# Optimization experiments

Hardware: AMD Instinct MI355X
Metric: run time of the kernel (lower is better)

The kernel has to match this reference:

```python
import jax, jax.numpy as jnp
import numpy as np

B, N, HD = 4, 2048, 256
E, T = 4096, 1024
PROPAG_STEPS = 5
ALPHA_MAX = 0.2
LN_EPS = 1e-5


def setup_inputs() -> dict:
    key = jax.random.key(0)
    ks = jax.random.split(key, 16)
    s_in, s_h = (2.0 * HD) ** -0.5, HD ** -0.5
    return {
        "attr_matrix": jax.random.normal(ks[0], (B, N, 1), dtype=jnp.float32),
        "adj_matrix": jax.random.uniform(ks[1], (B, N, N), dtype=jnp.float32),
        # ggnn.linear_i: 1 -> HD
        "W_i": jax.random.normal(ks[2], (HD, 1), dtype=jnp.float32),
        "b_i": jnp.zeros((HD,), dtype=jnp.float32),
        # ggnn.gru: GRUCell(input=2*HD, hidden=HD), torch gate order r,z,n
        "W_ih": jax.random.normal(ks[3], (3 * HD, 2 * HD), dtype=jnp.float32) * s_in,
        "b_ih": jnp.zeros((3 * HD,), dtype=jnp.float32),
        "W_hh": jax.random.normal(ks[4], (3 * HD, HD), dtype=jnp.float32) * s_h,
        "b_hh": jnp.zeros((3 * HD,), dtype=jnp.float32),
        # ggnn.linear_o: HD -> 1
        "W_o": jax.random.normal(ks[5], (1, HD), dtype=jnp.float32) * s_h,
        "b_o": jnp.zeros((1,), dtype=jnp.float32),
        # topo buffers (incidence-like, kept small to mimic sparse +/-1 matrices)
        "B1": jax.random.normal(ks[6], (N, E), dtype=jnp.float32) * 0.02,
        "B2": jax.random.normal(ks[7], (E, T), dtype=jnp.float32) * 0.02,
        # topo trainables
        "proj_W": jax.random.normal(ks[8], (HD, HD), dtype=jnp.float32) * s_h,
        "ln_gamma": jnp.ones((HD,), dtype=jnp.float32),
        "ln_beta": jnp.zeros((HD,), dtype=jnp.float32),
        "alpha_raw": jnp.float32(-2.0),
    }


def _gru_cell(x, h, W_ih, b_ih, W_hh, b_hh):
    # x: [B,N,2H], h: [B,N,H]; torch GRUCell gate order: r, z, n
    gx = jnp.einsum('bni,gi->bng', x, W_ih) + b_ih
    gh = jnp.einsum('bnh,gh->bng', h, W_hh) + b_hh
    xr, xz, xn = jnp.split(gx, 3, axis=-1)
    hr, hz, hn = jnp.split(gh, 3, axis=-1)
    r = jax.nn.sigmoid(xr + hr)
    z = jax.nn.sigmoid(xz + hz)
    n = jnp.tanh(xn + r * hn)
    return (1.0 - z) * n + z * h


def _layernorm(x, gamma, beta):
    mu = jnp.mean(x, axis=-1, keepdims=True)
    var = jnp.mean(jnp.square(x - mu), axis=-1, keepdims=True)
    return (x - mu) * jax.lax.rsqrt(var + LN_EPS) * gamma + beta


def reference(attr_matrix, adj_matrix, W_i, b_i, W_ih, b_ih, W_hh, b_hh,
              W_o, b_o, B1, B2, proj_W, ln_gamma, ln_beta, alpha_raw):
    A_in = adj_matrix                      # [B,N,N]
    A_out = jnp.swapaxes(adj_matrix, -2, -1)
    # linear_i + relu
    h = jax.nn.relu(jnp.einsum('bnc,hc->bnh', attr_matrix, W_i) + b_i)  # [B,N,H]
    # GGNN propagation
    for _ in range(PROPAG_STEPS):
        a_in = jnp.einsum('bnm,bmh->bnh', A_in, h)
        a_out = jnp.einsum('bnm,bmh->bnh', A_out, h)
        h = _gru_cell(jnp.concatenate((a_in, a_out), axis=-1), h,
                      W_ih, b_ih, W_hh, b_hh)
    # topo residual: dH = B1 (L1 (B1^T h)), L1 = B1^T B1 + B2 B2^T
    L1 = B1.T @ B1 + B2 @ B2.T             # [E,E]
    E_feat = jnp.einsum('ne,bnh->beh', B1, h)       # B1^T H
    E_topo = jnp.einsum('ef,bfh->beh', L1, E_feat)
    dH = jnp.einsum('ne,beh->bnh', B1, E_topo)
    dH = _layernorm(jax.nn.relu(jnp.einsum('bnh,oh->bno', dH, proj_W)),
                    ln_gamma, ln_beta)
    alpha = ALPHA_MAX * jax.nn.sigmoid(alpha_raw)
    h = h + alpha * dH
    # linear_o -> [B,N] (squeeze(0) is a no-op for B>1)
    anomaly = (jnp.einsum('bnh,oh->bno', h, W_o) + b_o)[..., 0]
    return anomaly
```

## Files before the change

### kernel.cpp

```cpp
#include <hip/hip_runtime.h>
#include <hip/hip_fp16.h>


typedef __bf16 bf16x8 __attribute__((ext_vector_type(8)));
typedef _Float16 f16x8 __attribute__((ext_vector_type(8)));
typedef float f32x4 __attribute__((ext_vector_type(4)));

#define BM 128
#define BN 128
#define BK 16
#define LO_INV (1.f / 1024.f)

__device__ __forceinline__ unsigned short bf16rne(float x)
{
    unsigned u = __float_as_uint(x);
    return (unsigned short)((u + 0x7FFFu + ((u >> 16) & 1u)) >> 16);
}
__device__ __forceinline__ float bf2f(unsigned short h)
{
    return __uint_as_float((unsigned)h << 16);
}
__device__ __forceinline__ void split2(float x, unsigned short& hi, unsigned short& lo)
{
    hi = bf16rne(x);
    lo = bf16rne(x - bf2f(hi));
}

__device__ __forceinline__ unsigned short f16r(float x)
{
    return __half_as_ushort(__float2half(x));
}
__device__ __forceinline__ float f16f(unsigned short u)
{
    return __half2float(__ushort_as_half(u));
}
__device__ __forceinline__ void splitf(float x, unsigned short& hi, unsigned short& lo)
{
    hi = f16r(x);
    lo = f16r((x - f16f(hi)) * 1024.f);
}

__device__ __forceinline__ void gload_lds16(const unsigned short* g, unsigned short* l)
{
    __builtin_amdgcn_global_load_lds(
        (const __attribute__((address_space(1))) void*)g,
        (__attribute__((address_space(3))) void*)l, 16, 0, 0);
}

__device__ __forceinline__ void stage2(const unsigned short* g, unsigned short* l, int ld)
{
    gload_lds16(g, l);
    gload_lds16(g + (size_t)32 * ld, l + 2048);
}

template<int SPLIT>
__device__ __forceinline__ void mm_loop64f(
    const unsigned short* ag0, const unsigned short* ag1,
    const unsigned short* bg0, const unsigned short* bg1,
    int K, int lda, int ldb, unsigned short* LDS, int tid,
    f32x4 (&acc0)[2][2], f32x4 (&acc1)[2][2])
{
    constexpr int NT = SPLIT ? 2 : 1;
    constexpr int TSZ = 4096;

    int lane = tid & 63, r16 = lane & 15, g = lane >> 4, s7 = r16 & 7;
    int wv = tid >> 6, wr = wv >> 1, wc = wv & 1;
    int arow = (wr * 32 + r16) * 128;
    int brow = (wc * 32 + r16) * 128;
    unsigned short* lA = LDS + (tid >> 6) * 512;
    unsigned short* lB = LDS + NT * TSZ + (tid >> 6) * 512;
    const char* Ab = (const char*)LDS;
    const char* Bb = (const char*)(LDS + NT * TSZ);

    for (int k0 = 0; k0 < K; k0 += 64) {
        stage2(ag0 + k0, lA, lda);
        if constexpr (SPLIT) stage2(ag1 + k0, lA + TSZ, lda);
        stage2(bg0 + k0, lB, ldb);
        if constexpr (SPLIT) stage2(bg1 + k0, lB + TSZ, ldb);
        __syncthreads();
#pragma unroll
        for (int ks = 0; ks < 2; ++ks) {
            int tt = ((ks * 4 + g) ^ s7) * 16;
            f16x8 a0[2], a1[2], b0[2], b1[2];
#pragma unroll
            for (int mi = 0; mi < 2; ++mi) {
                a0[mi] = *(const f16x8*)(Ab + arow + mi * 2048 + tt);
                if constexpr (SPLIT)
                    a1[mi] = *(const f16x8*)(Ab + TSZ * 2 + arow + mi * 2048 + tt);
            }
#pragma unroll
            for (int ni = 0; ni < 2; ++ni) {
                b0[ni] = *(const f16x8*)(Bb + brow + ni * 2048 + tt);
                if constexpr (SPLIT)
                    b1[ni] = *(const f16x8*)(Bb + TSZ * 2 + brow + ni * 2048 + tt);
            }
#pragma unroll
            for (int mi = 0; mi < 2; ++mi)
#pragma unroll
                for (int ni = 0; ni < 2; ++ni) {
                    if constexpr (SPLIT) {
                        acc1[mi][ni] = __builtin_amdgcn_mfma_f32_16x16x32_f16(
                            a1[mi], b0[ni], acc1[mi][ni], 0, 0, 0);
                        acc1[mi][ni] = __builtin_amdgcn_mfma_f32_16x16x32_f16(
                            a0[mi], b1[ni], acc1[mi][ni], 0, 0, 0);
                    }
                    acc0[mi][ni] = __builtin_amdgcn_mfma_f32_16x16x32_f16(
                        a0[mi], b0[ni], acc0[mi][ni], 0, 0, 0);
                }
        }
        __syncthreads();
    }
}

template<int SPLIT, int OF16>
__global__ __launch_bounds__(256, 2) void mm_f16(
    const unsigned short* __restrict__ Ah, const unsigned short* __restrict__ Al,
    int lda,
    const unsigned short* __restrict__ Bh, const unsigned short* __restrict__ Bl,
    int ldb,
    int K, const float* __restrict__ bias, const float* __restrict__ Cacc,
    void* __restrict__ Cout, int ldc)
{
    constexpr int NT = SPLIT ? 2 : 1;
    __shared__ unsigned short LDS[2 * NT * 4096];
    int tid = threadIdx.x;

    unsigned nwg = gridDim.x * gridDim.y;
    unsigned lin = blockIdx.y * gridDim.x + blockIdx.x;
    unsigned wk = ((nwg & 7) == 0) ? (lin & 7) * (nwg >> 3) + (lin >> 3) : lin;
    unsigned bx = wk % gridDim.x, by = wk / gridDim.x;

    int m0 = by * 64, n0 = bx * 64;
    int rp = tid >> 3, sl8 = ((tid & 7) ^ (rp & 7)) * 8;
    const unsigned short* ag0 = Ah + (size_t)(m0 + rp) * lda + sl8;
    const unsigned short* ag1 = SPLIT ? Al + (size_t)(m0 + rp) * lda + sl8 : nullptr;
    const unsigned short* bg0 = Bh + (size_t)(n0 + rp) * ldb + sl8;
    const unsigned short* bg1 = SPLIT ? Bl + (size_t)(n0 + rp) * ldb + sl8 : nullptr;

    f32x4 acc0[2][2], acc1[2][2];
#pragma unroll
    for (int mi = 0; mi < 2; ++mi)
#pragma unroll
        for (int ni = 0; ni < 2; ++ni) {
            acc0[mi][ni] = (f32x4){0.f, 0.f, 0.f, 0.f};
            acc1[mi][ni] = (f32x4){0.f, 0.f, 0.f, 0.f};
        }

    mm_loop64f<SPLIT>(ag0, ag1, bg0, bg1, K, lda, ldb, LDS, tid, acc0, acc1);

    int lane = tid & 63, r16 = lane & 15, g = lane >> 4;
    int wv = tid >> 6, wr = wv >> 1, wc = wv & 1;
#pragma unroll
    for (int mi = 0; mi < 2; ++mi) {
#pragma unroll
        for (int ni = 0; ni < 2; ++ni) {
            int col = n0 + wc * 32 + ni * 16 + r16;
            float badd = bias ? bias[col] : 0.f;
#pragma unroll
            for (int j = 0; j < 4; ++j) {
                int row = m0 + wr * 32 + mi * 16 + g * 4 + j;
                float v = acc0[mi][ni][j] + badd;
                if (SPLIT) v += acc1[mi][ni][j] * LO_INV;
                if (Cacc) v += Cacc[(size_t)row * ldc + col];
                if (OF16)
                    ((unsigned short*)Cout)[(size_t)row * ldc + col] = f16r(v);
                else
                    ((float*)Cout)[(size_t)row * ldc + col] = v;
            }
        }
    }
}

__global__ __launch_bounds__(256, 2) void gxgru(
    const unsigned short* __restrict__ Xhi, const unsigned short* __restrict__ Xlo,
    const unsigned short* __restrict__ WihH, const unsigned short* __restrict__ WihL,
    const float* __restrict__ b_ih, const float* __restrict__ ghb,
    float* __restrict__ h,
    unsigned short* __restrict__ hrmh, unsigned short* __restrict__ hrml,
    unsigned short* __restrict__ hTh, unsigned short* __restrict__ hTl)
{
    __shared__ unsigned short LDS[34816];
    int tid = threadIdx.x;

    unsigned lin = blockIdx.y * 4 + blockIdx.x;
    unsigned wk = (lin & 7) * 64 + (lin >> 3);
    unsigned tb = wk & 3, by = wk >> 2;

    int m0 = by * 64;
    const int K = 512;
    int rp = tid >> 3, sl8 = ((tid & 7) ^ (rp & 7)) * 8;
    const unsigned short* ag0 = Xhi + (size_t)(m0 + rp) * K + sl8;
    const unsigned short* ag1 = Xlo + (size_t)(m0 + rp) * K + sl8;
    const unsigned short* bh0 = WihH + (size_t)(tb * 192 + rp) * K + sl8;
    const unsigned short* bl0 = WihL + (size_t)(tb * 192 + rp) * K + sl8;

    int lane = tid & 63, r16 = lane & 15, lg = lane >> 4, s7 = r16 & 7;
    int wv = tid >> 6, wr = wv >> 1, wc = wv & 1;
    int arow = (wr * 32 + r16) * 128;
    int brow = (wc * 32 + r16) * 128;
    unsigned short* lA = LDS + (tid >> 6) * 512;
    unsigned short* lB = LDS + 8192 + (tid >> 6) * 512;

    f32x4 acc0[3][2][2], acc1[3][2][2];
#pragma unroll
    for (int g = 0; g < 3; ++g)
#pragma unroll
        for (int mi = 0; mi < 2; ++mi)
#pragma unroll
            for (int ni = 0; ni < 2; ++ni) {
                acc0[g][mi][ni] = (f32x4){0.f, 0.f, 0.f, 0.f};
                acc1[g][mi][ni] = (f32x4){0.f, 0.f, 0.f, 0.f};
            }

    for (int k0 = 0; k0 < K; k0 += 64) {
        stage2(ag0 + k0, lA, K);
        stage2(ag1 + k0, lA + 4096, K);
#pragma unroll
        for (int g = 0; g < 3; ++g) {
            stage2(bh0 + (size_t)(g * 64) * K + k0, lB + g * 4096, K);
            stage2(bl0 + (size_t)(g * 64) * K + k0, lB + 12288 + g * 4096, K);
        }
        __syncthreads();
#pragma unroll
        for (int ks = 0; ks < 2; ++ks) {
            int tt = ((ks * 4 + lg) ^ s7) * 16;
            f16x8 a0[2], a1[2];
#pragma unroll
            for (int mi = 0; mi < 2; ++mi) {
                a0[mi] = *(const f16x8*)((const char*)LDS + arow + mi * 2048 + tt);
                a1[mi] = *(const f16x8*)((const char*)LDS + 8192 + arow + mi * 2048 + tt);
            }
#pragma unroll
            for (int g = 0; g < 3; ++g) {
                f16x8 b0[2], b1[2];
#pragma unroll
                for (int ni = 0; ni < 2; ++ni) {
                    b0[ni] = *(const f16x8*)((const char*)LDS + 16384 + g * 8192 +
                                             brow + ni * 2048 + tt);
                    b1[ni] = *(const f16x8*)((const char*)LDS + 40960 + g * 8192 +
                                             brow + ni * 2048 + tt);
                }
#pragma unroll
                for (int mi = 0; mi < 2; ++mi)
#pragma unroll
                    for (int ni = 0; ni < 2; ++ni) {
                        acc1[g][mi][ni] = __builtin_amdgcn_mfma_f32_16x16x32_f16(
                            a1[mi], b0[ni], acc1[g][mi][ni], 0, 0, 0);
                        acc1[g][mi][ni] = __builtin_amdgcn_mfma_f32_16x16x32_f16(
                            a0[mi], b1[ni], acc1[g][mi][ni], 0, 0, 0);
                        acc0[g][mi][ni] = __builtin_amdgcn_mfma_f32_16x16x32_f16(
                            a0[mi], b0[ni], acc0[g][mi][ni], 0, 0, 0);
                    }
            }
        }
        __syncthreads();
    }

    float* T2 = reinterpret_cast<float*>(LDS);
#pragma unroll
    for (int mi = 0; mi < 2; ++mi) {
#pragma unroll
        for (int ni = 0; ni < 2; ++ni) {
            int tl = wc * 32 + ni * 16 + r16;
            int t = tb * 64 + tl;
            float br = b_ih[t], bz = b_ih[256 + t], bn = b_ih[512 + t];
#pragma unroll
            for (int j = 0; j < 4; ++j) {
                int rl = wr * 32 + mi * 16 + lg * 4 + j;
                int row = m0 + rl;
                float xr = acc0[0][mi][ni][j] + acc1[0][mi][ni][j] * LO_INV + br;
                float xz = acc0[1][mi][ni][j] + acc1[1][mi][ni][j] * LO_INV + bz;
                float xn = acc0[2][mi][ni][j] + acc1[2][mi][ni][j] * LO_INV + bn;
                size_t grow = (size_t)row * 768;
                float hr = ghb[grow + t];
                float hz = ghb[grow + 256 + t];
                float hn = ghb[grow + 512 + t];
                float r = 1.f / (1.f + __expf(-(xr + hr)));
                float z = 1.f / (1.f + __expf(-(xz + hz)));
                float nn = tanhf(xn + r * hn);
                size_t hix = (size_t)row * 256 + t;
                T2[rl * 68 + tl] = (1.f - z) * nn + z * h[hix];
            }
        }
    }
    __syncthreads();

    {
        int rl = tid >> 2, tq = tid & 3;
        const float* src = T2 + rl * 68 + tq * 16;
        int row = m0 + rl;
        int tbase = tb * 64 + tq * 16;
        unsigned hw[8], lw[8];
#pragma unroll
        for (int e = 0; e < 8; ++e) {
            unsigned short h0, l0, h1, l1;
            splitf(src[2 * e], h0, l0);
            splitf(src[2 * e + 1], h1, l1);
            hw[e] = (unsigned)h0 | ((unsigned)h1 << 16);
            lw[e] = (unsigned)l0 | ((unsigned)l1 << 16);
        }
        float* hd = h + (size_t)row * 256 + tbase;
#pragma unroll
        for (int q = 0; q < 4; ++q)
            ((float4*)hd)[q] = *(const float4*)(src + q * 4);
        size_t ro = (size_t)row * 256 + tbase;
        ((uint4*)(hrmh + ro))[0] = (uint4){hw[0], hw[1], hw[2], hw[3]};
        ((uint4*)(hrmh + ro))[1] = (uint4){hw[4], hw[5], hw[6], hw[7]};
        ((uint4*)(hrml + ro))[0] = (uint4){lw[0], lw[1], lw[2], lw[3]};
        ((uint4*)(hrml + ro))[1] = (uint4){lw[4], lw[5], lw[6], lw[7]};
    }

    {
        int b = tid >> 6, tl = tid & 63;
        int f = b * 256 + tb * 64 + tl;
        int nbase = m0 >> 2;
        unsigned hw[8], lw[8];
#pragma unroll
        for (int e = 0; e < 8; ++e) {
            float x0 = T2[(4 * (2 * e) + b) * 68 + tl];
            float x1 = T2[(4 * (2 * e + 1) + b) * 68 + tl];
            unsigned short h0, l0, h1, l1;
            splitf(x0, h0, l0);
            splitf(x1, h1, l1);
            hw[e] = (unsigned)h0 | ((unsigned)h1 << 16);
            lw[e] = (unsigned)l0 | ((unsigned)l1 << 16);
        }
        size_t fo = (size_t)f * 2048 + nbase;
        ((uint4*)(hTh + fo))[0] = (uint4){hw[0], hw[1], hw[2], hw[3]};
        ((uint4*)(hTh + fo))[1] = (uint4){hw[4], hw[5], hw[6], hw[7]};
        ((uint4*)(hTl + fo))[0] = (uint4){lw[0], lw[1], lw[2], lw[3]};
        ((uint4*)(hTl + fo))[1] = (uint4){lw[4], lw[5], lw[6], lw[7]};
    }
}

__global__ __launch_bounds__(256, 2) void mm_step1f(
    const unsigned short* __restrict__ AhHi, const unsigned short* __restrict__ AhLo,
    const unsigned short* __restrict__ AtHi, const unsigned short* __restrict__ AtLo,
    const unsigned short* __restrict__ hTh, const unsigned short* __restrict__ hTl,
    unsigned short* __restrict__ Xhi, unsigned short* __restrict__ Xlo,
    const unsigned short* __restrict__ hrmh, const unsigned short* __restrict__ hrml,
    const unsigned short* __restrict__ WhhH, const unsigned short* __restrict__ WhhL,
    const float* __restrict__ b_hh, float* __restrict__ ghb)
{
    __shared__ unsigned short LDS[16384];
    int tid = threadIdx.x;
    unsigned bid = blockIdx.x;
    int lane = tid & 63, r16 = lane & 15, g = lane >> 4;
    int wv = tid >> 6, wr = wv >> 1, wc = wv & 1;
    int rp = tid >> 3, sl8 = ((tid & 7) ^ (rp & 7)) * 8;

    f32x4 acc0[2][2], acc1[2][2];
#pragma unroll
    for (int mi = 0; mi < 2; ++mi)
#pragma unroll
        for (int ni = 0; ni < 2; ++ni) {
            acc0[mi][ni] = (f32x4){0.f, 0.f, 0.f, 0.f};
            acc1[mi][ni] = (f32x4){0.f, 0.f, 0.f, 0.f};
        }

    if (bid < 1024) {
        unsigned wk = (bid & 7) * 128 + (bid >> 3);
        unsigned bz = wk >> 7, rem = wk & 127, by = rem >> 2, bx = rem & 3;
        int b = bz >> 1, wio = bz & 1;
        const unsigned short* Ahp = (wio ? AtHi : AhHi) + (size_t)b * 4194304;
        const unsigned short* Alp = (wio ? AtLo : AhLo) + (size_t)b * 4194304;
        size_t boff = (size_t)(b * 256 + bx * 64) * 2048;
        int m0 = by * 64;
        const int K = 2048;
        const unsigned short* ag0 = Ahp + (size_t)(m0 + rp) * K + sl8;
        const unsigned short* ag1 = Alp + (size_t)(m0 + rp) * K + sl8;
        const unsigned short* bg0 = hTh + boff + (size_t)rp * K + sl8;
        const unsigned short* bg1 = hTl + boff + (size_t)rp * K + sl8;

        mm_loop64f<1>(ag0, ag1, bg0, bg1, K, K, K, LDS, tid, acc0, acc1);

        float* T = reinterpret_cast<float*>(LDS);
#pragma unroll
        for (int mi = 0; mi < 2; ++mi)
#pragma unroll
            for (int ni = 0; ni < 2; ++ni)
#pragma unroll
                for (int j = 0; j < 4; ++j)
                    T[(wr * 32 + mi * 16 + g * 4 + j) * 68 +
                      wc * 32 + ni * 16 + r16] =
                        acc0[mi][ni][j] + acc1[mi][ni][j] * LO_INV;
        __syncthreads();

        int row = tid >> 2, fq = tid & 3;
        const float* src = T + row * 68 + fq * 16;
        unsigned hw[8], lw[8];
#pragma unroll
        for (int e = 0; e < 8; ++e) {
            unsigned short h0, l0, h1, l1;
            splitf(src[2 * e], h0, l0);
            splitf(src[2 * e + 1], h1, l1);
            hw[e] = (unsigned)h0 | ((unsigned)h1 << 16);
            lw[e] = (unsigned)l0 | ((unsigned)l1 << 16);
        }
        size_t base = ((size_t)(m0 + row) * 4 + b) * 512 + wio * 256 + bx * 64 + fq * 16;
        ((uint4*)(Xhi + base))[0] = (uint4){hw[0], hw[1], hw[2], hw[3]};
        ((uint4*)(Xhi + base))[1] = (uint4){hw[4], hw[5], hw[6], hw[7]};
        ((uint4*)(Xlo + base))[0] = (uint4){lw[0], lw[1], lw[2], lw[3]};
        ((uint4*)(Xlo + base))[1] = (uint4){lw[4], lw[5], lw[6], lw[7]};
    } else {
        unsigned gidx = bid - 1024;
        unsigned by = gidx / 12, bx = gidx % 12;
        int m0 = by * 64, n0 = bx * 64;
        const int K = 256;
        const unsigned short* ag0 = hrmh + (size_t)(m0 + rp) * K + sl8;
        const unsigned short* ag1 = hrml + (size_t)(m0 + rp) * K + sl8;
        const unsigned short* bg0 = WhhH + (size_t)(n0 + rp) * K + sl8;
        const unsigned short* bg1 = WhhL + (size_t)(n0 + rp) * K + sl8;

        mm_loop64f<1>(ag0, ag1, bg0, bg1, K, K, K, LDS, tid, acc0, acc1);

#pragma unroll
        for (int mi = 0; mi < 2; ++mi) {
#pragma unroll
            for (int ni = 0; ni < 2; ++ni) {
                int col = n0 + wc * 32 + ni * 16 + r16;
                float badd = b_hh[col];
#pragma unroll
                for (int j = 0; j < 4; ++j) {
                    int row = m0 + wr * 32 + mi * 16 + g * 4 + j;
                    ghb[(size_t)row * 768 + col] =
                        acc0[mi][ni][j] + acc1[mi][ni][j] * LO_INV + badd;
                }
            }
        }
    }
}

__global__ void split_adj16(const float* __restrict__ adj,
                            unsigned short* __restrict__ nhi, unsigned short* __restrict__ nlo,
                            unsigned short* __restrict__ thi, unsigned short* __restrict__ tlo)
{
    __shared__ float t[64][68];
    int z = blockIdx.z;
    const float* src = adj + (size_t)z * 4194304;
    int tx = threadIdx.x & 15, ty = threadIdx.x >> 4;
    int i0 = blockIdx.y * 64, j0 = blockIdx.x * 64;
#pragma unroll
    for (int i = 0; i < 4; ++i) {
        int r = ty * 4 + i;
        float4 v = *(const float4*)(src + (size_t)(i0 + r) * 2048 + j0 + tx * 4);
        ushort4 h, l;
        splitf(v.x, h.x, l.x); splitf(v.y, h.y, l.y);
        splitf(v.z, h.z, l.z); splitf(v.w, h.w, l.w);
        size_t o = (size_t)z * 4194304 + (size_t)(i0 + r) * 2048 + j0 + tx * 4;
        *(ushort4*)(nhi + o) = h; *(ushort4*)(nlo + o) = l;
        t[r][tx * 4 + 0] = v.x; t[r][tx * 4 + 1] = v.y;
        t[r][tx * 4 + 2] = v.z; t[r][tx * 4 + 3] = v.w;
    }
    __syncthreads();
#pragma unroll
    for (int i = 0; i < 4; ++i) {
        int r = ty * 4 + i;
        ushort4 h, l;
        splitf(t[tx * 4 + 0][r], h.x, l.x);
        splitf(t[tx * 4 + 1][r], h.y, l.y);
        splitf(t[tx * 4 + 2][r], h.z, l.z);
        splitf(t[tx * 4 + 3][r], h.w, l.w);
        size_t o = (size_t)z * 4194304 + (size_t)(j0 + r) * 2048 + i0 + tx * 4;
        *(ushort4*)(thi + o) = h; *(ushort4*)(tlo + o) = l;
    }
}

__global__ void split_h16(const float* __restrict__ h,
                          unsigned short* __restrict__ hi, unsigned short* __restrict__ lo,
                          unsigned short* __restrict__ hrmh, unsigned short* __restrict__ hrml)
{
    __shared__ float t[64][68];
    int f0 = blockIdx.x * 64, n0 = blockIdx.y * 64;
    int tx = threadIdx.x & 15, ty = threadIdx.x >> 4;
#pragma unroll
    for (int i = 0; i < 4; ++i) {
        int r = ty * 4 + i;
        float4 v = *(const float4*)(h + (size_t)(n0 + r) * 1024 + f0 + tx * 4);
        t[r][tx * 4 + 0] = v.x; t[r][tx * 4 + 1] = v.y;
        t[r][tx * 4 + 2] = v.z; t[r][tx * 4 + 3] = v.w;
        if (hrmh) {
            ushort4 hh, ll;
            splitf(v.x, hh.x, ll.x); splitf(v.y, hh.y, ll.y);
            splitf(v.z, hh.z, ll.z); splitf(v.w, hh.w, ll.w);
            size_t o = (size_t)(n0 + r) * 1024 + f0 + tx * 4;
            *(ushort4*)(hrmh + o) = hh;
            *(ushort4*)(hrml + o) = ll;
        }
    }
    __syncthreads();
#pragma unroll
    for (int i = 0; i < 4; ++i) {
        int r = ty * 4 + i;
        ushort4 hh, ll;
        splitf(t[tx * 4 + 0][r], hh.x, ll.x);
        splitf(t[tx * 4 + 1][r], hh.y, ll.y);
        splitf(t[tx * 4 + 2][r], hh.z, ll.z);
        splitf(t[tx * 4 + 3][r], hh.w, ll.w);
        size_t o = (size_t)(f0 + r) * 2048 + n0 + tx * 4;
        *(ushort4*)(hi + o) = hh; *(ushort4*)(lo + o) = ll;
    }
}

__global__ void split_t16(const float* __restrict__ in,
                          unsigned short* __restrict__ outN, int ldN,
                          unsigned short* __restrict__ outT, int ldT,
                          int R, int C)
{
    __shared__ float t[64][68];
    int i0 = blockIdx.y * 64, j0 = blockIdx.x * 64;
    int tx = threadIdx.x & 15, ty = threadIdx.x >> 4;
#pragma unroll
    for (int i = 0; i < 4; ++i) {
        int r = ty * 4 + i;
        float4 v = *(const float4*)(in + (size_t)(i0 + r) * C + j0 + tx * 4);
        ushort4 hh;
        hh.x = f16r(v.x); hh.y = f16r(v.y);
        hh.z = f16r(v.z); hh.w = f16r(v.w);
        *(ushort4*)(outN + (size_t)(i0 + r) * ldN + j0 + tx * 4) = hh;
        t[r][tx * 4 + 0] = v.x; t[r][tx * 4 + 1] = v.y;
        t[r][tx * 4 + 2] = v.z; t[r][tx * 4 + 3] = v.w;
    }
    __syncthreads();
#pragma unroll
    for (int i = 0; i < 4; ++i) {
        int r = ty * 4 + i;
        ushort4 hh;
        hh.x = f16r(t[tx * 4 + 0][r]);
        hh.y = f16r(t[tx * 4 + 1][r]);
        hh.z = f16r(t[tx * 4 + 2][r]);
        hh.w = f16r(t[tx * 4 + 3][r]);
        *(ushort4*)(outT + (size_t)(j0 + r) * ldT + i0 + tx * 4) = hh;
    }
}

__global__ void split_w16(const float* __restrict__ Wih, const float* __restrict__ Whh,
                          const float* __restrict__ pj,
                          unsigned short* __restrict__ WihH, unsigned short* __restrict__ WihL,
                          unsigned short* __restrict__ WhhH, unsigned short* __restrict__ WhhL,
                          unsigned short* __restrict__ pjH)
{
    int i = blockIdx.x * 256 + threadIdx.x;
    if (i < 393216) {
        int row = i >> 9, col = i & 511;
        int g = row >> 8, t = row & 255;
        int nrow = (t >> 6) * 192 + g * 64 + (t & 63);
        unsigned short h, l;
        splitf(Wih[i], h, l);
        WihH[nrow * 512 + col] = h; WihL[nrow * 512 + col] = l;
    } else if (i < 589824) {
        int j = i - 393216;
        unsigned short h, l;
        splitf(Whh[j], h, l);
        WhhH[j] = h; WhhL[j] = l;
    } else if (i < 655360) {
        int j = i - 589824;
        pjH[j] = f16r(pj[j]);
    }
}

__global__ __launch_bounds__(256, 2) void gemm_f32(
    const float* __restrict__ A, const float* __restrict__ B, float* __restrict__ C,
    int M, int N, int K, int lda, int ldb, int ldc,
    long sA, long sB, long sC,
    const float* __restrict__ bias, int ta, int tb, int accum)
{
    int bz = blockIdx.z;
    int taEff = ta;
    if (ta == 2) {
        int b = bz >> 1, w = bz & 1;
        A += (long)b * sA; B += (long)b * sB; C += (long)b * sC + w * 256;
        taEff = w;
    } else {
        A += (long)bz * sA; B += (long)bz * sB; C += (long)bz * sC;
    }
    int m0 = blockIdx.y * BM, n0 = blockIdx.x * BN;

    __shared__ float As[BK][BM + 4];
    __shared__ float Bs[BK][BN + 4];

    int tid = threadIdx.x;
    int tx = tid & 15, ty = tid >> 4;

    float acc[64];
#pragma unroll
    for (int i = 0; i < 64; ++i) acc[i] = 0.f;

    for (int k0 = 0; k0 < K; k0 += BK) {
        if (!taEff) {
            int m = tid >> 1, kk = (tid & 1) * 8;
            const float* src = A + (long)(m0 + m) * lda + (k0 + kk);
            float4 v0 = *(const float4*)(src);
            float4 v1 = *(const float4*)(src + 4);
            As[kk + 0][m] = v0.x; As[kk + 1][m] = v0.y;
            As[kk + 2][m] = v0.z; As[kk + 3][m] = v0.w;
            As[kk + 4][m] = v1.x; As[kk + 5][m] = v1.y;
            As[kk + 6][m] = v1.z; As[kk + 7][m] = v1.w;
        } else {
            int k = tid >> 4, mm = (tid & 15) * 8;
            const float* src = A + (long)(k0 + k) * lda + (m0 + mm);
            *(float4*)&As[k][mm]     = *(const float4*)(src);
            *(float4*)&As[k][mm + 4] = *(const float4*)(src + 4);
        }
        if (!tb) {
            int k = tid >> 4, nn = (tid & 15) * 8;
            const float* src = B + (long)(k0 + k) * ldb + (n0 + nn);
            *(float4*)&Bs[k][nn]     = *(const float4*)(src);
            *(float4*)&Bs[k][nn + 4] = *(const float4*)(src + 4);
        } else {
            int n = tid >> 1, kk = (tid & 1) * 8;
            const float* src = B + (long)(n0 + n) * ldb + (k0 + kk);
            float4 v0 = *(const float4*)(src);
            float4 v1 = *(const float4*)(src + 4);
            Bs[kk + 0][n] = v0.x; Bs[kk + 1][n] = v0.y;
            Bs[kk + 2][n] = v0.z; Bs[kk + 3][n] = v0.w;
            Bs[kk + 4][n] = v1.x; Bs[kk + 5][n] = v1.y;
            Bs[kk + 6][n] = v1.z; Bs[kk + 7][n] = v1.w;
        }
        __syncthreads();

#pragma unroll
        for (int k = 0; k < BK; ++k) {
            float a[8], b[8];
            *(float4*)&a[0] = *(const float4*)&As[k][ty * 4];
            *(float4*)&a[4] = *(const float4*)&As[k][64 + ty * 4];
            *(float4*)&b[0] = *(const float4*)&Bs[k][tx * 4];
            *(float4*)&b[4] = *(const float4*)&Bs[k][64 + tx * 4];
#pragma unroll
            for (int i = 0; i < 8; ++i)
#pragma unroll
                for (int j = 0; j < 8; ++j)
                    acc[i * 8 + j] += a[i] * b[j];
        }
        __syncthreads();
    }

#pragma unroll
    for (int i = 0; i < 8; ++i) {
        int row = m0 + ((i >> 2) ? 64 : 0) + ty * 4 + (i & 3);
#pragma unroll
        for (int jh = 0; jh < 2; ++jh) {
            int col = n0 + jh * 64 + tx * 4;
            float4 v;
            v.x = acc[i * 8 + jh * 4 + 0];
            v.y = acc[i * 8 + jh * 4 + 1];
            v.z = acc[i * 8 + jh * 4 + 2];
            v.w = acc[i * 8 + jh * 4 + 3];
            if (bias) {
                v.x += bias[col + 0]; v.y += bias[col + 1];
                v.z += bias[col + 2]; v.w += bias[col + 3];
            }
            float* dst = C + (long)row * ldc + col;
            if (accum) {
                float4 o = *(const float4*)dst;
                v.x += o.x; v.y += o.y; v.z += o.z; v.w += o.w;
            }
            *(float4*)dst = v;
        }
    }
}

__global__ void split_adj(const float* __restrict__ adj,
                          unsigned short* __restrict__ nhi, unsigned short* __restrict__ nlo,
                          unsigned short* __restrict__ thi, unsigned short* __restrict__ tlo)
{
    __shared__ float t[64][68];
    int z = blockIdx.z;
    const float* src = adj + (size_t)z * 4194304;
    int tx = threadIdx.x & 15, ty = threadIdx.x >> 4;
    int i0 = blockIdx.y * 64, j0 = blockIdx.x * 64;
#pragma unroll
    for (int i = 0; i < 4; ++i) {
        int r = ty * 4 + i;
        float4 v = *(const float4*)(src + (size_t)(i0 + r) * 2048 + j0 + tx * 4);
        ushort4 h, l;
        split2(v.x, h.x, l.x); split2(v.y, h.y, l.y);
        split2(v.z, h.z, l.z); split2(v.w, h.w, l.w);
        size_t o = (size_t)z * 4194304 + (size_t)(i0 + r) * 2048 + j0 + tx * 4;
        *(ushort4*)(nhi + o) = h; *(ushort4*)(nlo + o) = l;
        t[r][tx * 4 + 0] = v.x; t[r][tx * 4 + 1] = v.y;
        t[r][tx * 4 + 2] = v.z; t[r][tx * 4 + 3] = v.w;
    }
    __syncthreads();
#pragma unroll
    for (int i = 0; i < 4; ++i) {
        int r = ty * 4 + i;
        ushort4 h, l;
        split2(t[tx * 4 + 0][r], h.x, l.x);
        split2(t[tx * 4 + 1][r], h.y, l.y);
        split2(t[tx * 4 + 2][r], h.z, l.z);
        split2(t[tx * 4 + 3][r], h.w, l.w);
        size_t o = (size_t)z * 4194304 + (size_t)(j0 + r) * 2048 + i0 + tx * 4;
        *(ushort4*)(thi + o) = h; *(ushort4*)(tlo + o) = l;
    }
}

__global__ void split_h(const float* __restrict__ h,
                        unsigned short* __restrict__ hi, unsigned short* __restrict__ lo)
{
    __shared__ float t[64][68];
    int f0 = blockIdx.x * 64, n0 = blockIdx.y * 64;
    int tx = threadIdx.x & 15, ty = threadIdx.x >> 4;
#pragma unroll
    for (int i = 0; i < 4; ++i) {
        int r = ty * 4 + i;
        float4 v = *(const float4*)(h + (size_t)(n0 + r) * 1024 + f0 + tx * 4);
        t[r][tx * 4 + 0] = v.x; t[r][tx * 4 + 1] = v.y;
        t[r][tx * 4 + 2] = v.z; t[r][tx * 4 + 3] = v.w;
    }
    __syncthreads();
#pragma unroll
    for (int i = 0; i < 4; ++i) {
        int r = ty * 4 + i;
        ushort4 hh, ll;
        split2(t[tx * 4 + 0][r], hh.x, ll.x);
        split2(t[tx * 4 + 1][r], hh.y, ll.y);
        split2(t[tx * 4 + 2][r], hh.z, ll.z);
        split2(t[tx * 4 + 3][r], hh.w, ll.w);
        size_t o = (size_t)(f0 + r) * 2048 + n0 + tx * 4;
        *(ushort4*)(hi + o) = hh; *(ushort4*)(lo + o) = ll;
    }
}

__global__ __launch_bounds__(256, 3) void adj_mfma(
    const unsigned short* __restrict__ AhHi, const unsigned short* __restrict__ AhLo,
    const unsigned short* __restrict__ AtHi, const unsigned short* __restrict__ AtLo,
    const unsigned short* __restrict__ hTHi, const unsigned short* __restrict__ hTLo,
    float* __restrict__ c0, float* __restrict__ c1, float* __restrict__ c2)
{
    __shared__ unsigned short As[8192];
    __shared__ unsigned short Bs[8192];
    int tid = threadIdx.x;
    int bz = blockIdx.z;
    int region = bz >> 3, bw = bz & 7, b = bw >> 1, w = bw & 1;
    const unsigned short* Abase =
        (region == 2) ? (w ? AtLo : AhLo) : (w ? AtHi : AhHi);
    Abase += (size_t)b * 4194304;
    const unsigned short* Bbase = (region == 1) ? hTLo : hTHi;
    float* Cb = (region == 0) ? c0 : (region == 1 ? c1 : c2);

    int m0 = blockIdx.y * 128;
    int f0 = b * 256 + blockIdx.x * 128;

    int rp = tid >> 3;
    int sl = (tid & 7) ^ (rp & 7);
    const unsigned short* ag = Abase + (size_t)(m0 + rp) * 2048 + sl * 8;
    const unsigned short* bg = Bbase + (size_t)(f0 + rp) * 2048 + sl * 8;
    unsigned short* al = &As[(tid >> 6) * 512];
    unsigned short* bl = &Bs[(tid >> 6) * 512];

    int lane = tid & 63, r16 = lane & 15, g = lane >> 4;
    int wv = tid >> 6, wr = wv >> 1, wc = wv & 1;
    int s7 = r16 & 7;
    int t0 = (g ^ s7) * 16, t1 = ((4 + g) ^ s7) * 16;
    int arow = (wr * 64 + r16) * 128;
    int brow = (wc * 64 + r16) * 128;

    f32x4 acc[4][4];
#pragma unroll
    for (int mi = 0; mi < 4; ++mi)
#pragma unroll
        for (int ni = 0; ni < 4; ++ni)
            acc[mi][ni] = (f32x4){0.f, 0.f, 0.f, 0.f};

    for (int k0 = 0; k0 < 2048; k0 += 64) {
#pragma unroll
        for (int i = 0; i < 4; ++i)
            gload_lds16(ag + k0 + (size_t)i * 65536, al + i * 2048);
#pragma unroll
        for (int i = 0; i < 4; ++i)
            gload_lds16(bg + k0 + (size_t)i * 65536, bl + i * 2048);
        __syncthreads();

#pragma unroll
        for (int ks = 0; ks < 2; ++ks) {
            int tt = ks ? t1 : t0;
            bf16x8 af[4], bf[4];
#pragma unroll
            for (int mi = 0; mi < 4; ++mi)
                af[mi] = *(const bf16x8*)((const char*)As + arow + mi * 2048 + tt);
#pragma unroll
            for (int ni = 0; ni < 4; ++ni)
                bf[ni] = *(const bf16x8*)((const char*)Bs + brow + ni * 2048 + tt);
#pragma unroll
            for (int mi = 0; mi < 4; ++mi)
#pragma unroll
                for (int ni = 0; ni < 4; ++ni)
                    acc[mi][ni] = __builtin_amdgcn_mfma_f32_16x16x32_bf16(
                        af[mi], bf[ni], acc[mi][ni], 0, 0, 0);
        }
        __syncthreads();
    }

    int cbase = b * 512 + w * 256 + blockIdx.x * 128 + wc * 64;
#pragma unroll
    for (int mi = 0; mi < 4; ++mi) {
        int row = m0 + wr * 64 + mi * 16 + g * 4;
#pragma unroll
        for (int ni = 0; ni < 4; ++ni) {
            int col = cbase + ni * 16 + r16;
            float* dst = Cb + (size_t)row * 2048 + col;
#pragma unroll
            for (int j = 0; j < 4; ++j) dst[(size_t)j * 2048] = acc[mi][ni][j];
        }
    }
}

__global__ void reduce3(float4* __restrict__ x, const float4* __restrict__ p,
                        const float4* __restrict__ q)
{
    int i = blockIdx.x * 256 + threadIdx.x;
    float4 a = x[i], b = p[i], c = q[i];
    a.x += b.x + c.x; a.y += b.y + c.y; a.z += b.z + c.z; a.w += b.w + c.w;
    x[i] = a;
}

__global__ void init_h(const float* __restrict__ attr, const float* __restrict__ W_i,
                       const float* __restrict__ b_i, float* __restrict__ h)
{
    int n = blockIdx.x, b = blockIdx.y, t = threadIdx.x;
    float a = attr[b * 2048 + n];
    h[(long)n * 1024 + b * 256 + t] = fmaxf(a * W_i[t] + b_i[t], 0.f);
}

__global__ void gru_ew(const float* __restrict__ gx, const float* __restrict__ gh,
                       float* __restrict__ h)
{
    int n = blockIdx.x, b = blockIdx.y, t = threadIdx.x;
    long row = ((long)n * 4 + b) * 768;
    float xr = gx[row + t], xz = gx[row + 256 + t], xn = gx[row + 512 + t];
    float hr = gh[row + t], hz = gh[row + 256 + t], hn = gh[row + 512 + t];
    float r = 1.f / (1.f + __expf(-(xr + hr)));
    float z = 1.f / (1.f + __expf(-(xz + hz)));
    float nn = tanhf(xn + r * hn);
    long hi = (long)n * 1024 + b * 256 + t;
    float ho = h[hi];
    h[hi] = (1.f - z) * nn + z * ho;
}

__global__ void ln_out(const float* __restrict__ dP, const float* __restrict__ gamma,
                       const float* __restrict__ beta, const float* __restrict__ araw,
                       const float* __restrict__ h, const float* __restrict__ W_o,
                       const float* __restrict__ b_o, float* __restrict__ out)
{
    int n = blockIdx.x, b = blockIdx.y, t = threadIdx.x;
    long row = ((long)n * 4 + b) * 256;
    float v = fmaxf(dP[row + t], 0.f);
    float s = v, s2 = v * v;
#pragma unroll
    for (int o = 1; o < 64; o <<= 1) { s += __shfl_xor(s, o); s2 += __shfl_xor(s2, o); }
    __shared__ float red[8];
    int w = t >> 6, lane = t & 63;
    if (lane == 0) { red[w] = s; red[4 + w] = s2; }
    __syncthreads();
    float S  = red[0] + red[1] + red[2] + red[3];
    float S2 = red[4] + red[5] + red[6] + red[7];
    float mu = S * (1.f / 256.f);
    float var = S2 * (1.f / 256.f) - mu * mu;
    float rs = rsqrtf(var + 1e-5f);
    float alpha = 0.2f / (1.f + __expf(-araw[0]));
    float y = h[(long)n * 1024 + b * 256 + t] +
              alpha * ((v - mu) * rs * gamma[t] + beta[t]);
    float d = y * W_o[t];
#pragma unroll
    for (int o = 1; o < 64; o <<= 1) d += __shfl_xor(d, o);
    __syncthreads();
    if (lane == 0) red[w] = d;
    __syncthreads();
    if (t == 0) out[(long)b * 2048 + n] = red[0] + red[1] + red[2] + red[3] + b_o[0];
}

__global__ void ln_residual(const float* __restrict__ dP, const float* __restrict__ gamma,
                            const float* __restrict__ beta, const float* __restrict__ araw,
                            float* __restrict__ h)
{
    int n = blockIdx.x, b = blockIdx.y, t = threadIdx.x;
    long row = ((long)n * 4 + b) * 256;
    float v = fmaxf(dP[row + t], 0.f);
    float s = v, s2 = v * v;
#pragma unroll
    for (int o = 1; o < 64; o <<= 1) { s += __shfl_xor(s, o); s2 += __shfl_xor(s2, o); }
    __shared__ float red[8];
    int w = t >> 6, lane = t & 63;
    if (lane == 0) { red[w] = s; red[4 + w] = s2; }
    __syncthreads();
    float S  = red[0] + red[1] + red[2] + red[3];
    float S2 = red[4] + red[5] + red[6] + red[7];
    float mu = S * (1.f / 256.f);
    float var = S2 * (1.f / 256.f) - mu * mu;
    float rs = rsqrtf(var + 1e-5f);
    float alpha = 0.2f / (1.f + __expf(-araw[0]));
    long hi = (long)n * 1024 + b * 256 + t;
    h[hi] += alpha * ((v - mu) * rs * gamma[t] + beta[t]);
}

__global__ void out_kernel(const float* __restrict__ h, const float* __restrict__ W_o,
                           const float* __restrict__ b_o, float* __restrict__ out)
{
    int t = threadIdx.x;
    int w = t >> 6, lane = t & 63;
    int row = blockIdx.x * 4 + w;
    int n = row >> 2, b = row & 3;
    const float* hp = h + (long)n * 1024 + b * 256;
    float s = 0.f;
#pragma unroll
    for (int i = 0; i < 4; ++i) { int c = i * 64 + lane; s += hp[c] * W_o[c]; }
#pragma unroll
    for (int o = 1; o < 64; o <<= 1) s += __shfl_xor(s, o);
    if (lane == 0) out[(long)b * 2048 + n] = s + b_o[0];
}

extern "C" void kernel_launch(void* const* d_in, const int* in_sizes, int n_in,
                              void* d_out, int out_size, void* d_ws, size_t ws_size,
                              hipStream_t stream)
{
    (void)in_sizes; (void)n_in; (void)out_size;
    const float* attr  = (const float*)d_in[0];
    const float* adj   = (const float*)d_in[1];
    const float* W_i   = (const float*)d_in[2];
    const float* b_i   = (const float*)d_in[3];
    const float* W_ih  = (const float*)d_in[4];
    const float* b_ih  = (const float*)d_in[5];
    const float* W_hh  = (const float*)d_in[6];
    const float* b_hh  = (const float*)d_in[7];
    const float* W_o   = (const float*)d_in[8];
    const float* b_o   = (const float*)d_in[9];
    const float* B1    = (const float*)d_in[10];
    const float* B2    = (const float*)d_in[11];
    const float* projW = (const float*)d_in[12];
    const float* gamma = (const float*)d_in[13];
    const float* beta  = (const float*)d_in[14];
    const float* araw  = (const float*)d_in[15];
    float* out = (float*)d_out;

    char* wsb = (char*)d_ws;
    dim3 blk(256);

    const size_t REQ1 = 0xD400000;
    const size_t REQ2 = 0xD000000;

    if (ws_size >= REQ1) {
        float* hbuf = (float*)(wsb);
        unsigned short* hrmh = (unsigned short*)(wsb + 0x0800000);
        unsigned short* hrml = (unsigned short*)(wsb + 0x0C00000);
        unsigned short* hTh  = (unsigned short*)(wsb + 0x1800000);
        unsigned short* hTl  = (unsigned short*)(wsb + 0x1C00000);
        float* ghb  = (float*)(wsb + 0x2000000);
        unsigned short* Xhi = (unsigned short*)(wsb + 0x3800000);
        unsigned short* Xlo = (unsigned short*)(wsb + 0x4000000);
        unsigned short* Wih_h = (unsigned short*)(wsb + 0x5000000);
        unsigned short* Wih_l = (unsigned short*)(wsb + 0x50C0000);
        unsigned short* Whh_h = (unsigned short*)(wsb + 0x5240000);
        unsigned short* Whh_l = (unsigned short*)(wsb + 0x52A0000);
        unsigned short* pjh   = (unsigned short*)(wsb + 0x5300000);
        char* R1 = wsb + 0x5400000;
        unsigned short* AhHi = (unsigned short*)(R1);
        unsigned short* AhLo = (unsigned short*)(R1 + 0x2000000);
        unsigned short* AtHi = (unsigned short*)(R1 + 0x4000000);
        unsigned short* AtLo = (unsigned short*)(R1 + 0x6000000);
        unsigned short* B1h  = (unsigned short*)(R1);
        unsigned short* B2T  = (unsigned short*)(R1 + 0x1000000);
        unsigned short* uTb  = (unsigned short*)(R1 + 0x1800000);
        unsigned short* prT  = (unsigned short*)(R1 + 0x2000000);
        unsigned short* qTb  = (unsigned short*)(R1 + 0x2600000);
        unsigned short* Bcat = (unsigned short*)(R1 + 0x2E00000);
        unsigned short* dHb  = (unsigned short*)(wsb + 0x1800000);
        float* dPb = ghb;

        init_h<<<dim3(2048, 4), blk, 0, stream>>>(attr, W_i, b_i, hbuf);
        split_adj16<<<dim3(32, 32, 4), blk, 0, stream>>>(adj, AhHi, AhLo, AtHi, AtLo);
        split_w16<<<dim3(2560), blk, 0, stream>>>(W_ih, W_hh, projW,
            Wih_h, Wih_l, Whh_h, Whh_l, pjh);
        split_h16<<<dim3(16, 32), blk, 0, stream>>>(hbuf, hTh, hTl, hrmh, hrml);

        for (int step = 0; step < 5; ++step) {
            mm_step1f<<<dim3(2560), blk, 0, stream>>>(
                AhHi, AhLo, AtHi, AtLo, hTh, hTl, Xhi, Xlo,
                hrmh, hrml, Whh_h, Whh_l, b_hh, ghb);
            gxgru<<<dim3(4, 128), blk, 0, stream>>>(
                Xhi, Xlo, Wih_h, Wih_l, b_ih, ghb, hbuf,
                hrmh, hrml, hTh, hTl);
        }

        split_t16<<<dim3(64, 32), blk, 0, stream>>>(B1, B1h, 4096, Bcat, 3072,
                                                    2048, 4096);
        split_t16<<<dim3(16, 64), blk, 0, stream>>>(B2, Bcat + 2048, 3072, B2T, 4096,
                                                    4096, 1024);
        mm_f16<0, 1><<<dim3(64, 16), blk, 0, stream>>>(
            hTh, nullptr, 2048, Bcat, nullptr, 3072,
            2048, nullptr, nullptr, uTb, 4096);
        mm_f16<0, 1><<<dim3(48, 16), blk, 0, stream>>>(
            uTb, nullptr, 4096, B1h, nullptr, 4096,
            4096, nullptr, nullptr, prT, 3072);
        mm_f16<0, 1><<<dim3(64, 16), blk, 0, stream>>>(
            prT, nullptr, 3072, Bcat, nullptr, 3072,
            3072, nullptr, nullptr, qTb, 4096);
        mm_f16<0, 1><<<dim3(16, 32), blk, 0, stream>>>(
            B1h, nullptr, 4096, qTb, nullptr, 4096,
            4096, nullptr, nullptr, dHb, 1024);
        mm_f16<0, 0><<<dim3(4, 128), blk, 0, stream>>>(
            dHb, nullptr, 256, pjh, nullptr, 256,
            256, nullptr, nullptr, dPb, 256);

        ln_out<<<dim3(2048, 4), blk, 0, stream>>>(dPb, gamma, beta, araw,
                                                  hbuf, W_o, b_o, out);
        return;
    }

    float* hbuf = (float*)(wsb);
    float* xbuf = (float*)(wsb + 0x800000);
    float* gxb  = (float*)(wsb + 0x1800000);
    float* ghb  = (float*)(wsb + 0x3000000);
    unsigned short* AhHi = (unsigned short*)(wsb + 0x4800000);
    unsigned short* AhLo = (unsigned short*)(wsb + 0x6800000);
    unsigned short* AtHi = (unsigned short*)(wsb + 0x8800000);
    unsigned short* AtLo = (unsigned short*)(wsb + 0xA800000);
    unsigned short* hTHi = (unsigned short*)(wsb + 0xC800000);
    unsigned short* hTLo = (unsigned short*)(wsb + 0xCC00000);

    float* ub  = xbuf;
    float* pb  = gxb;
    float* qb  = gxb + (1 << 21);
    float* rb  = ghb;
    float* dHr = ghb + (1 << 20);
    float* dPb = ghb + 3 * (1 << 20);

    bool mfma_path = (ws_size >= REQ2);

    init_h<<<dim3(2048, 4), blk, 0, stream>>>(attr, W_i, b_i, hbuf);

    if (mfma_path)
        split_adj<<<dim3(32, 32, 4), blk, 0, stream>>>(adj, AhHi, AhLo, AtHi, AtLo);

    for (int step = 0; step < 5; ++step) {
        if (mfma_path) {
            split_h<<<dim3(16, 32), blk, 0, stream>>>(hbuf, hTHi, hTLo);
            adj_mfma<<<dim3(2, 16, 24), blk, 0, stream>>>(
                AhHi, AhLo, AtHi, AtLo, hTHi, hTLo, xbuf, gxb, ghb);
            reduce3<<<dim3(4096), blk, 0, stream>>>(
                (float4*)xbuf, (const float4*)gxb, (const float4*)ghb);
        } else {
            gemm_f32<<<dim3(2, 16, 8), blk, 0, stream>>>(
                adj, hbuf, xbuf, 2048, 256, 2048, 2048, 1024, 2048,
                (long)2048 * 2048, 256, 512, nullptr, 2, 0, 0);
        }
        gemm_f32<<<dim3(6, 64, 1), blk, 0, stream>>>(
            xbuf, W_ih, gxb, 8192, 768, 512, 512, 512, 768,
            0, 0, 0, b_ih, 0, 1, 0);
        gemm_f32<<<dim3(6, 64, 1), blk, 0, stream>>>(
            hbuf, W_hh, ghb, 8192, 768, 256, 256, 256, 768,
            0, 0, 0, b_hh, 0, 1, 0);
        gru_ew<<<dim3(2048, 4), blk, 0, stream>>>(gxb, ghb, hbuf);
    }

    gemm_f32<<<dim3(8, 32, 1), blk, 0, stream>>>(
        B1, hbuf, ub, 4096, 1024, 2048, 4096, 1024, 1024, 0, 0, 0, nullptr, 1, 0, 0);
    gemm_f32<<<dim3(8, 16, 1), blk, 0, stream>>>(
        B1, ub, pb, 2048, 1024, 4096, 4096, 1024, 1024, 0, 0, 0, nullptr, 0, 0, 0);
    gemm_f32<<<dim3(8, 32, 1), blk, 0, stream>>>(
        B1, pb, qb, 4096, 1024, 2048, 4096, 1024, 1024, 0, 0, 0, nullptr, 1, 0, 0);
    gemm_f32<<<dim3(8, 8, 1), blk, 0, stream>>>(
        B2, ub, rb, 1024, 1024, 4096, 1024, 1024, 1024, 0, 0, 0, nullptr, 1, 0, 0);
    gemm_f32<<<dim3(8, 32, 1), blk, 0, stream>>>(
        B2, rb, qb, 4096, 1024, 1024, 1024, 1024, 1024, 0, 0, 0, nullptr, 0, 0, 1);
    gemm_f32<<<dim3(8, 16, 1), blk, 0, stream>>>(
        B1, qb, dHr, 2048, 1024, 4096, 4096, 1024, 1024, 0, 0, 0, nullptr, 0, 0, 0);
    gemm_f32<<<dim3(2, 64, 1), blk, 0, stream>>>(
        dHr, projW, dPb, 8192, 256, 256, 256, 256, 256, 0, 0, 0, nullptr, 0, 1, 0);

    ln_residual<<<dim3(2048, 4), blk, 0, stream>>>(dPb, gamma, beta, araw, hbuf);
    out_kernel<<<dim3(2048), blk, 0, stream>>>(hbuf, W_o, b_o, out);
}
```

Before: 744.8 us.

## Double-buffer LDS in the f16 split GEMM loop with async prefetch

Converts the single-buffered global_load_lds k-loop into a two-stage pipeline: the next two k-tiles are issued up front, and each iteration waits only on the older tile's loads (vmcnt) before computing, then refills the freed buffer. The aim is to overlap global-to-LDS traffic with MFMA work instead of stalling on every tile. LDS allocation doubles, which may reduce occupancy under launch_bounds(256,2), and a barrier is added before the epilogue reuses LDS.

Measured after the change: 758.1 us. No clear change (+1.8%).

```diff
diff --git a/kernel.cpp b/kernel.cpp
--- a/kernel.cpp
+++ b/kernel.cpp
@@ -46,6 +46,16 @@
         (const __attribute__((address_space(1))) void*)g,
         (__attribute__((address_space(3))) void*)l, 16, 0, 0);
 }
+
+template<int N>
+__device__ __forceinline__ void waitcnt_vm()
+{
+    if constexpr (N == 0)      asm volatile("s_waitcnt vmcnt(0)" ::: "memory");
+    else if constexpr (N == 4) asm volatile("s_waitcnt vmcnt(4)" ::: "memory");
+    else if constexpr (N == 8) asm volatile("s_waitcnt vmcnt(8)" ::: "memory");
+    else                       asm volatile("s_waitcnt vmcnt(0)" ::: "memory");
+}
+__device__ __forceinline__ void cfence() { asm volatile("" ::: "memory"); }
 
 __device__ __forceinline__ void stage2(const unsigned short* g, unsigned short* l, int ld)
 {
@@ -62,22 +72,37 @@
 {
     constexpr int NT = SPLIT ? 2 : 1;
     constexpr int TSZ = 4096;
+    constexpr int BUF = 2 * NT * TSZ;
+    constexpr int NL = 4 * NT;
 
     int lane = tid & 63, r16 = lane & 15, g = lane >> 4, s7 = r16 & 7;
     int wv = tid >> 6, wr = wv >> 1, wc = wv & 1;
     int arow = (wr * 32 + r16) * 128;
     int brow = (wc * 32 + r16) * 128;
-    unsigned short* lA = LDS + (tid >> 6) * 512;
-    unsigned short* lB = LDS + NT * TSZ + (tid >> 6) * 512;
-    const char* Ab = (const char*)LDS;
-    const char* Bb = (const char*)(LDS + NT * TSZ);
-
-    for (int k0 = 0; k0 < K; k0 += 64) {
-        stage2(ag0 + k0, lA, lda);
-        if constexpr (SPLIT) stage2(ag1 + k0, lA + TSZ, lda);
-        stage2(bg0 + k0, lB, ldb);
-        if constexpr (SPLIT) stage2(bg1 + k0, lB + TSZ, ldb);
-        __syncthreads();
+    int wslot = (tid >> 6) * 512;
+
+    int nK = K >> 6;
+
+    auto STAGE = [&](int buf, int k0) {
+        unsigned short* base = LDS + buf * BUF;
+        stage2(ag0 + k0, base + wslot, lda);
+        if constexpr (SPLIT) stage2(ag1 + k0, base + TSZ + wslot, lda);
+        stage2(bg0 + k0, base + NT * TSZ + wslot, ldb);
+        if constexpr (SPLIT) stage2(bg1 + k0, base + NT * TSZ + TSZ + wslot, ldb);
+    };
+
+    STAGE(0, 0);
+    if (nK > 1) STAGE(1, 64);
+
+    for (int k = 0; k < nK; ++k) {
+        if (k < nK - 1) waitcnt_vm<NL>();
+        else            waitcnt_vm<0>();
+        cfence();
+        __builtin_amdgcn_s_barrier();
+        cfence();
+
+        const char* Ab = (const char*)(LDS + (k & 1) * BUF);
+        const char* Bb = Ab + NT * TSZ * 2;
 #pragma unroll
         for (int ks = 0; ks < 2; ++ks) {
             int tt = ((ks * 4 + g) ^ s7) * 16;
@@ -108,7 +133,11 @@
                         a0[mi], b0[ni], acc0[mi][ni], 0, 0, 0);
                 }
         }
-        __syncthreads();
+
+        cfence();
+        __builtin_amdgcn_s_barrier();
+        cfence();
+        if (k + 2 < nK) STAGE(k & 1, (k + 2) * 64);
     }
 }
 
@@ -122,7 +151,7 @@
     void* __restrict__ Cout, int ldc)
 {
     constexpr int NT = SPLIT ? 2 : 1;
-    __shared__ unsigned short LDS[2 * NT * 4096];
+    __shared__ unsigned short LDS[4 * NT * 4096];
     int tid = threadIdx.x;
 
     unsigned nwg = gridDim.x * gridDim.y;
@@ -342,7 +371,7 @@
     const unsigned short* __restrict__ WhhH, const unsigned short* __restrict__ WhhL,
     const float* __restrict__ b_hh, float* __restrict__ ghb)
 {
-    __shared__ unsigned short LDS[16384];
+    __shared__ unsigned short LDS[32768];
     int tid = threadIdx.x;
     unsigned bid = blockIdx.x;
     int lane = tid & 63, r16 = lane & 15, g = lane >> 4;
@@ -373,6 +402,7 @@
         const unsigned short* bg1 = hTl + boff + (size_t)rp * K + sl8;
 
         mm_loop64f<1>(ag0, ag1, bg0, bg1, K, K, K, LDS, tid, acc0, acc1);
+        __syncthreads();
 
         float* T = reinterpret_cast<float*>(LDS);
 #pragma unroll
```
